# Kernel optimization log

Hardware: AMD Instinct MI355X
Metric: run time of the kernel (lower is better)

The kernel has to match this reference:

```python
import jax, jax.numpy as jnp
import numpy as np

B, N, D_IN = 256, 64, 128   # batch, n_agents, input_dim
H0, H1, H2 = 256, 256, 64   # rnn_hidden_dim[0], [1], [2]


def setup_inputs() -> dict:
    key = jax.random.key(0)
    ks = jax.random.split(key, 14)
    s = 0.05
    return {
        "obs": jax.random.normal(ks[0], (B, N, D_IN), dtype=jnp.float32),
        "W_enc": jax.random.normal(ks[1], (H0, D_IN), dtype=jnp.float32) * s,
        "b_enc": jax.random.normal(ks[2], (H0,), dtype=jnp.float32) * s,
        "W_obs": jax.random.normal(ks[3], (H0, H0), dtype=jnp.float32) * s,
        "b_obs": jax.random.normal(ks[4], (H0,), dtype=jnp.float32) * s,
        "W_ih": jax.random.normal(ks[5], (3 * H0, H0), dtype=jnp.float32) * s,
        "b_ih": jax.random.normal(ks[6], (3 * H0,), dtype=jnp.float32) * s,
        "W_hh": jax.random.normal(ks[7], (3 * H0, H0), dtype=jnp.float32) * s,
        "b_hh": jax.random.normal(ks[8], (3 * H0,), dtype=jnp.float32) * s,
        "W_val": jax.random.normal(ks[9], (H1, H0), dtype=jnp.float32) * s,
        "b_val": jax.random.normal(ks[10], (H1,), dtype=jnp.float32) * s,
        "W_dec": jax.random.normal(ks[11], (H2, H1), dtype=jnp.float32) * s,
        "b_dec": jax.random.normal(ks[12], (H2,), dtype=jnp.float32) * s,
    }


def reference(obs, W_enc, b_enc, W_obs, b_obs, W_ih, b_ih, W_hh, b_hh,
              W_val, b_val, W_dec, b_dec):
    # encoding + f_obs  -> h: [B, N, H0]
    x = jax.nn.relu(jnp.einsum("bnd,hd->bnh", obs, W_enc) + b_enc)
    h = jnp.einsum("bnh,gh->bng", x, W_obs) + b_obs

    # comm: mean over other agents. Original masks self and divides by N
    # (mean over dim of size N with self zeroed) => (sum_all - self) / N.
    c = (jnp.sum(h, axis=1, keepdims=True) - h) / N  # [B, N, H0]

    # GRUCell(input=c, hidden=h), PyTorch gate ordering r, z, n
    gi = jnp.einsum("bnh,gh->bng", c, W_ih) + b_ih   # [B, N, 3*H0]
    gh = jnp.einsum("bnh,gh->bng", h, W_hh) + b_hh
    gi_r, gi_z, gi_n = jnp.split(gi, 3, axis=-1)
    gh_r, gh_z, gh_n = jnp.split(gh, 3, axis=-1)
    r = jax.nn.sigmoid(gi_r + gh_r)
    z = jax.nn.sigmoid(gi_z + gh_z)
    n = jnp.tanh(gi_n + r * gh_n)
    h = (1.0 - z) * n + z * h  # [B, N, H0]

    # value head + decoding; seq_len=1 squeezed -> [B, N, H2]
    v = jnp.einsum("bnh,vh->bnv", h, W_val) + b_val
    out = jnp.einsum("bnv,ov->bno", v, W_dec) + b_dec
    return out
```

## Files before the change

kernel.cpp:

```cpp
#include <hip/hip_runtime.h>
#include <hip/hip_bf16.h>
#include <math.h>


typedef __bf16  bf16x8 __attribute__((ext_vector_type(8)));
typedef float   f32x4  __attribute__((ext_vector_type(4)));

#define DIN 128
#define H0  256
#define SW  264
#define SWO 136
#define LOG2E 1.44269504088896f

#define O_WENC  0
#define O_WOBS  32768
#define O_WIH   98304
#define O_WHH   294912
#define O_WFUSE 491520
#define W_CONV  491520
#define NBLK_CONV 240
#define O_BFUSE_B 1015808

__device__ __forceinline__ f32x4 mfma16(bf16x8 a, bf16x8 b, f32x4 c) {
    return __builtin_amdgcn_mfma_f32_16x16x32_bf16(a, b, c, 0, 0, 0);
}
__device__ __forceinline__ float bf2f(__hip_bfloat16 x) { return __bfloat162float(x); }
__device__ __forceinline__ __hip_bfloat16 f2bf(float x) { return __float2bfloat16(x); }

__device__ __forceinline__ float fsigmoid(float x) {
    float e = __builtin_amdgcn_exp2f(-LOG2E * x);
    return __builtin_amdgcn_rcpf(1.0f + e);
}
__device__ __forceinline__ float ftanh(float x) {
    float e = __builtin_amdgcn_exp2f(2.0f * LOG2E * x);
    return 1.0f - 2.0f * __builtin_amdgcn_rcpf(1.0f + e);
}

__device__ __forceinline__ bf16x8 w8(const __hip_bfloat16* p, int idx) {
    return *(const bf16x8*)(p + idx);
}

__device__ __forceinline__ int tadr(int r, int k) { return r * SW + k; }
__device__ __forceinline__ int oadr(int r, int k) { return r * SWO + k; }

__global__ __launch_bounds__(256) void prep_kernel(
    const float* __restrict__ W_enc, const float* __restrict__ W_obs,
    const float* __restrict__ W_ih,  const float* __restrict__ W_hh,
    const float* __restrict__ W_val, const float* __restrict__ W_dec,
    const float* __restrict__ b_val, const float* __restrict__ b_dec,
    __hip_bfloat16* __restrict__ ws)
{
    const int blk = blockIdx.x;
    const int tid = threadIdx.x;
    if (blk < NBLK_CONV) {
        const int i = (blk * 256 + tid) * 8;
        const float* src; int off;
        if      (i < O_WOBS) { src = W_enc; off = O_WENC; }
        else if (i < O_WIH)  { src = W_obs; off = O_WOBS; }
        else if (i < O_WHH)  { src = W_ih;  off = O_WIH;  }
        else                 { src = W_hh;  off = O_WHH;  }
        const float* f = src + (i - off);
        f32x4 a = *(const f32x4*)f;
        f32x4 b = *(const f32x4*)(f + 4);
        bf16x8 v;
        #pragma unroll
        for (int j = 0; j < 4; j++) { v[j] = (__bf16)a[j]; v[j + 4] = (__bf16)b[j]; }
        *(bf16x8*)(ws + i) = v;
    } else {
        const int o = blk - NBLK_CONV;
        __shared__ float wd[256];
        wd[tid] = W_dec[o * 256 + tid];
        __syncthreads();
        float acc = 0.0f;
        #pragma unroll 16
        for (int v = 0; v < 256; v++)
            acc += wd[v] * W_val[v * 256 + tid];
        ws[O_WFUSE + o * 256 + tid] = f2bf(acc);
        if (tid < 64) {
            float p = 0.0f;
            #pragma unroll
            for (int v = tid; v < 256; v += 64) p += wd[v] * b_val[v];
            p += __shfl_xor(p, 32); p += __shfl_xor(p, 16); p += __shfl_xor(p, 8);
            p += __shfl_xor(p, 4);  p += __shfl_xor(p, 2);  p += __shfl_xor(p, 1);
            if (tid == 0) {
                float* bf = (float*)((char*)ws + O_BFUSE_B);
                bf[o] = p + b_dec[o];
            }
        }
    }
}

__global__ __launch_bounds__(512, 2) void commnet_mfma(
    const __hip_bfloat16* __restrict__ ws,
    const float* __restrict__ b_enc, const float* __restrict__ b_obs,
    const float* __restrict__ b_ih,  const float* __restrict__ b_hh,
    const float* __restrict__ obs,   float* __restrict__ out)
{
    __shared__ __align__(16) __hip_bfloat16 T0[64 * SW];
    __shared__ __align__(16) __hip_bfloat16 T1[64 * SW];

    const __hip_bfloat16* W_enc  = ws + O_WENC;
    const __hip_bfloat16* W_obs  = ws + O_WOBS;
    const __hip_bfloat16* W_ih   = ws + O_WIH;
    const __hip_bfloat16* W_hh   = ws + O_WHH;
    const __hip_bfloat16* W_fuse = ws + O_WFUSE;
    const float* b_fuse = (const float*)((const char*)ws + O_BFUSE_B);

    const int tid  = threadIdx.x;
    const int wave = tid >> 6;
    const int lane = tid & 63;
    const int quad = lane >> 4;
    const int lc   = lane & 15;
    const int row0 = blockIdx.x * 64;
    const int ko16 = quad * 8;

    for (int i = tid; i < 64 * DIN / 8; i += 512) {
        const int r = i >> 4;
        const int c = (i & 15) << 3;
        const float* src = obs + (row0 + r) * DIN + c;
        f32x4 a = *(const f32x4*)src;
        f32x4 b = *(const f32x4*)(src + 4);
        bf16x8 v;
        #pragma unroll
        for (int j = 0; j < 4; j++) { v[j] = (__bf16)a[j]; v[j + 4] = (__bf16)b[j]; }
        *(bf16x8*)&T1[oadr(r, c)] = v;
    }
    __syncthreads();

    #pragma unroll
    for (int cp = 0; cp < 2; cp++) {
        const int n = (wave + 8 * cp) * 16 + lc;
        const float bias = b_enc[n];
        f32x4 acc[4] = {};
        #pragma unroll
        for (int k0 = 0; k0 < DIN; k0 += 32) {
            const int kk = k0 + ko16;
            bf16x8 b = w8(W_enc, n * DIN + kk);
            #pragma unroll
            for (int rt = 0; rt < 4; rt++) {
                bf16x8 a = *(const bf16x8*)&T1[oadr(rt * 16 + lc, kk)];
                acc[rt] = mfma16(a, b, acc[rt]);
            }
        }
        #pragma unroll
        for (int rt = 0; rt < 4; rt++)
            #pragma unroll
            for (int i = 0; i < 4; i++) {
                const int row = rt * 16 + quad * 4 + i;
                T0[tadr(row, n)] = f2bf(fmaxf(acc[rt][i] + bias, 0.0f));
            }
    }
    __syncthreads();

    #pragma unroll
    for (int cp = 0; cp < 2; cp++) {
        const int n = (wave + 8 * cp) * 16 + lc;
        const float bias = b_obs[n];
        f32x4 acc[4] = {};
        #pragma unroll
        for (int k0 = 0; k0 < H0; k0 += 32) {
            const int kk = k0 + ko16;
            bf16x8 b = w8(W_obs, n * H0 + kk);
            #pragma unroll
            for (int rt = 0; rt < 4; rt++) {
                bf16x8 a = *(const bf16x8*)&T0[tadr(rt * 16 + lc, kk)];
                acc[rt] = mfma16(a, b, acc[rt]);
            }
        }
        #pragma unroll
        for (int rt = 0; rt < 4; rt++)
            #pragma unroll
            for (int i = 0; i < 4; i++) {
                const int row = rt * 16 + quad * 4 + i;
                T1[tadr(row, n)] = f2bf(acc[rt][i] + bias);
            }
    }
    __syncthreads();

    #pragma unroll
    for (int cp = 0; cp < 2; cp++) {
        const int n = (wave + 8 * cp) * 16 + lc;
        const float bir = b_ih[n], biz = b_ih[n + 256], bin = b_ih[n + 512];
        const float bhr = b_hh[n], bhz = b_hh[n + 256], bhn = b_hh[n + 512];
        f32x4 gir[4] = {}, giz[4] = {}, gin[4] = {};
        f32x4 ghr[4] = {}, ghz[4] = {}, ghn[4] = {};
        #pragma unroll
        for (int k0 = 0; k0 < H0; k0 += 32) {
            const int kk = k0 + ko16;
            bf16x8 bir8 = w8(W_ih, (n      ) * H0 + kk);
            bf16x8 biz8 = w8(W_ih, (n + 256) * H0 + kk);
            bf16x8 bin8 = w8(W_ih, (n + 512) * H0 + kk);
            bf16x8 bhr8 = w8(W_hh, (n      ) * H0 + kk);
            bf16x8 bhz8 = w8(W_hh, (n + 256) * H0 + kk);
            bf16x8 bhn8 = w8(W_hh, (n + 512) * H0 + kk);
            #pragma unroll
            for (int rt = 0; rt < 4; rt++) {
                bf16x8 aH = *(const bf16x8*)&T1[tadr(rt * 16 + lc, kk)];
                gir[rt] = mfma16(aH, bir8, gir[rt]);
                giz[rt] = mfma16(aH, biz8, giz[rt]);
                gin[rt] = mfma16(aH, bin8, gin[rt]);
                ghr[rt] = mfma16(aH, bhr8, ghr[rt]);
                ghz[rt] = mfma16(aH, bhz8, ghz[rt]);
                ghn[rt] = mfma16(aH, bhn8, ghn[rt]);
            }
        }
        float Sr = 0.0f, Sz = 0.0f, Sn = 0.0f;
        #pragma unroll
        for (int rt = 0; rt < 4; rt++)
            #pragma unroll
            for (int i = 0; i < 4; i++) {
                Sr += gir[rt][i]; Sz += giz[rt][i]; Sn += gin[rt][i];
            }
        Sr += __shfl_xor(Sr, 16); Sr += __shfl_xor(Sr, 32);
        Sz += __shfl_xor(Sz, 16); Sz += __shfl_xor(Sz, 32);
        Sn += __shfl_xor(Sn, 16); Sn += __shfl_xor(Sn, 32);

        #pragma unroll
        for (int rt = 0; rt < 4; rt++)
            #pragma unroll
            for (int i = 0; i < 4; i++) {
                const int row = rt * 16 + quad * 4 + i;
                const float gi_r = (Sr - gir[rt][i]) * (1.0f / 64.0f) + bir;
                const float gi_z = (Sz - giz[rt][i]) * (1.0f / 64.0f) + biz;
                const float gi_n = (Sn - gin[rt][i]) * (1.0f / 64.0f) + bin;
                const float r  = fsigmoid(gi_r + ghr[rt][i] + bhr);
                const float z  = fsigmoid(gi_z + ghz[rt][i] + bhz);
                const float nn = ftanh(gi_n + r * (ghn[rt][i] + bhn));
                const float h  = bf2f(T1[tadr(row, n)]);
                T0[tadr(row, n)] = f2bf((1.0f - z) * nn + z * h);
            }
    }
    __syncthreads();

    {
        const int ct  = wave & 3;
        const int rtb = (wave >> 2) * 2;
        const int nd  = ct * 16 + lc;
        const float bias = b_fuse[nd];
        f32x4 acc[2] = {};
        #pragma unroll
        for (int k0 = 0; k0 < H0; k0 += 32) {
            const int kk = k0 + ko16;
            bf16x8 b = w8(W_fuse, nd * H0 + kk);
            #pragma unroll
            for (int j = 0; j < 2; j++) {
                bf16x8 a = *(const bf16x8*)&T0[tadr((rtb + j) * 16 + lc, kk)];
                acc[j] = mfma16(a, b, acc[j]);
            }
        }
        #pragma unroll
        for (int j = 0; j < 2; j++)
            #pragma unroll
            for (int i = 0; i < 4; i++) {
                const int row = (rtb + j) * 16 + quad * 4 + i;
                out[(row0 + row) * 64 + nd] = acc[j][i] + bias;
            }
    }
}

extern "C" void kernel_launch(void* const* d_in, const int* in_sizes, int n_in,
                              void* d_out, int out_size, void* d_ws, size_t ws_size,
                              hipStream_t stream) {
    (void)in_sizes; (void)n_in; (void)out_size; (void)ws_size;
    const float* obs   = (const float*)d_in[0];
    const float* W_enc = (const float*)d_in[1];  const float* b_enc = (const float*)d_in[2];
    const float* W_obs = (const float*)d_in[3];  const float* b_obs = (const float*)d_in[4];
    const float* W_ih  = (const float*)d_in[5];  const float* b_ih  = (const float*)d_in[6];
    const float* W_hh  = (const float*)d_in[7];  const float* b_hh  = (const float*)d_in[8];
    const float* W_val = (const float*)d_in[9];  const float* b_val = (const float*)d_in[10];
    const float* W_dec = (const float*)d_in[11]; const float* b_dec = (const float*)d_in[12];
    float* out = (float*)d_out;
    __hip_bfloat16* ws = (__hip_bfloat16*)d_ws;

    prep_kernel<<<NBLK_CONV + 64, 256, 0, stream>>>(
        W_enc, W_obs, W_ih, W_hh, W_val, W_dec, b_val, b_dec, ws);
    commnet_mfma<<<256, 512, 0, stream>>>(
        ws, b_enc, b_obs, b_ih, b_hh, obs, out);
}
```

Measured before the change: 126.5 us.

## Split fused kernel into two half-batch kernels exchanging h through workspace

The single 256-block kernel becomes two kernels with 512 blocks, each block handling 32 of a batch's 64 agents. Kernel A runs encoder and f_obs, writes h and per-half column sums to global workspace. Kernel B rebuilds the comm term from the column sums: it computes W_ih times the summed h as a scalar dot product and combines it with per-row W_ih·h, so the agent mean no longer needs all 64 rows in one block. This doubles block count for better CU occupancy, at the cost of an extra launch, a global round trip of h, and reloading weights twice as often per row.

New measurement: 194.5 us. 53.8% more time.

```diff
diff --git a/kernel.cpp b/kernel.cpp
--- a/kernel.cpp
+++ b/kernel.cpp
@@ -17,9 +17,10 @@
 #define O_WIH   98304
 #define O_WHH   294912
 #define O_WFUSE 491520
-#define W_CONV  491520
 #define NBLK_CONV 240
 #define O_BFUSE_B 1015808
+#define O_CS_B    1016320
+#define O_H_B     1540608
 
 __device__ __forceinline__ f32x4 mfma16(bf16x8 a, bf16x8 b, f32x4 c) {
     return __builtin_amdgcn_mfma_f32_16x16x32_bf16(a, b, c, 0, 0, 0);
@@ -90,39 +91,38 @@
     }
 }
 
-__global__ __launch_bounds__(512, 2) void commnet_mfma(
-    const __hip_bfloat16* __restrict__ ws,
+__global__ __launch_bounds__(512, 2) void commnet_a(
+    __hip_bfloat16* __restrict__ ws,
     const float* __restrict__ b_enc, const float* __restrict__ b_obs,
-    const float* __restrict__ b_ih,  const float* __restrict__ b_hh,
-    const float* __restrict__ obs,   float* __restrict__ out)
+    const float* __restrict__ obs)
 {
-    __shared__ __align__(16) __hip_bfloat16 T0[64 * SW];
-    __shared__ __align__(16) __hip_bfloat16 T1[64 * SW];
-
-    const __hip_bfloat16* W_enc  = ws + O_WENC;
-    const __hip_bfloat16* W_obs  = ws + O_WOBS;
-    const __hip_bfloat16* W_ih   = ws + O_WIH;
-    const __hip_bfloat16* W_hh   = ws + O_WHH;
-    const __hip_bfloat16* W_fuse = ws + O_WFUSE;
-    const float* b_fuse = (const float*)((const char*)ws + O_BFUSE_B);
+    __shared__ __align__(16) __hip_bfloat16 T0[32 * SW];
+    __shared__ __align__(16) __hip_bfloat16 T1[32 * SW];
+
+    const __hip_bfloat16* W_enc = ws + O_WENC;
+    const __hip_bfloat16* W_obs = ws + O_WOBS;
+    float* cs = (float*)((char*)ws + O_CS_B);
+    __hip_bfloat16* Hb = (__hip_bfloat16*)((char*)ws + O_H_B);
 
     const int tid  = threadIdx.x;
     const int wave = tid >> 6;
     const int lane = tid & 63;
     const int quad = lane >> 4;
     const int lc   = lane & 15;
-    const int row0 = blockIdx.x * 64;
+    const int b    = blockIdx.x >> 1;
+    const int half = blockIdx.x & 1;
+    const int r0g  = b * 64 + half * 32;
     const int ko16 = quad * 8;
 
-    for (int i = tid; i < 64 * DIN / 8; i += 512) {
-        const int r = i >> 4;
-        const int c = (i & 15) << 3;
-        const float* src = obs + (row0 + r) * DIN + c;
+    {
+        const int r = tid >> 4;
+        const int c = (tid & 15) << 3;
+        const float* src = obs + (r0g + r) * DIN + c;
         f32x4 a = *(const f32x4*)src;
-        f32x4 b = *(const f32x4*)(src + 4);
+        f32x4 bq = *(const f32x4*)(src + 4);
         bf16x8 v;
         #pragma unroll
-        for (int j = 0; j < 4; j++) { v[j] = (__bf16)a[j]; v[j + 4] = (__bf16)b[j]; }
+        for (int j = 0; j < 4; j++) { v[j] = (__bf16)a[j]; v[j + 4] = (__bf16)bq[j]; }
         *(bf16x8*)&T1[oadr(r, c)] = v;
     }
     __syncthreads();
@@ -131,19 +131,19 @@
     for (int cp = 0; cp < 2; cp++) {
         const int n = (wave + 8 * cp) * 16 + lc;
         const float bias = b_enc[n];
-        f32x4 acc[4] = {};
+        f32x4 acc[2] = {};
         #pragma unroll
         for (int k0 = 0; k0 < DIN; k0 += 32) {
             const int kk = k0 + ko16;
-            bf16x8 b = w8(W_enc, n * DIN + kk);
-            #pragma unroll
-            for (int rt = 0; rt < 4; rt++) {
+            bf16x8 bw = w8(W_enc, n * DIN + kk);
+            #pragma unroll
+            for (int rt = 0; rt < 2; rt++) {
                 bf16x8 a = *(const bf16x8*)&T1[oadr(rt * 16 + lc, kk)];
-                acc[rt] = mfma16(a, b, acc[rt]);
-            }
-        }
-        #pragma unroll
-        for (int rt = 0; rt < 4; rt++)
+                acc[rt] = mfma16(a, bw, acc[rt]);
+            }
+        }
+        #pragma unroll
+        for (int rt = 0; rt < 2; rt++)
             #pragma unroll
             for (int i = 0; i < 4; i++) {
                 const int row = rt * 16 + quad * 4 + i;
@@ -156,35 +156,101 @@
     for (int cp = 0; cp < 2; cp++) {
         const int n = (wave + 8 * cp) * 16 + lc;
         const float bias = b_obs[n];
-        f32x4 acc[4] = {};
-        #pragma unroll
+        f32x4 acc[2] = {};
+        #pragma unroll 4
         for (int k0 = 0; k0 < H0; k0 += 32) {
             const int kk = k0 + ko16;
-            bf16x8 b = w8(W_obs, n * H0 + kk);
-            #pragma unroll
-            for (int rt = 0; rt < 4; rt++) {
+            bf16x8 bw = w8(W_obs, n * H0 + kk);
+            #pragma unroll
+            for (int rt = 0; rt < 2; rt++) {
                 bf16x8 a = *(const bf16x8*)&T0[tadr(rt * 16 + lc, kk)];
-                acc[rt] = mfma16(a, b, acc[rt]);
-            }
-        }
-        #pragma unroll
-        for (int rt = 0; rt < 4; rt++)
+                acc[rt] = mfma16(a, bw, acc[rt]);
+            }
+        }
+        float Sc = 0.0f;
+        #pragma unroll
+        for (int rt = 0; rt < 2; rt++)
             #pragma unroll
             for (int i = 0; i < 4; i++) {
                 const int row = rt * 16 + quad * 4 + i;
-                T1[tadr(row, n)] = f2bf(acc[rt][i] + bias);
-            }
-    }
+                const __hip_bfloat16 hb = f2bf(acc[rt][i] + bias);
+                T1[tadr(row, n)] = hb;
+                Sc += bf2f(hb);
+            }
+        Sc += __shfl_xor(Sc, 16); Sc += __shfl_xor(Sc, 32);
+        if (lane < 16) cs[blockIdx.x * 256 + n] = Sc;
+    }
+    __syncthreads();
+
+    for (int i = tid; i < 32 * H0 / 8; i += 512) {
+        const int r = i >> 5;
+        const int c = (i & 31) << 3;
+        *(bf16x8*)&Hb[(r0g + r) * H0 + c] = *(const bf16x8*)&T1[tadr(r, c)];
+    }
+}
+
+__global__ __launch_bounds__(512, 2) void commnet_b(
+    __hip_bfloat16* __restrict__ ws,
+    const float* __restrict__ b_ih, const float* __restrict__ b_hh,
+    float* __restrict__ out)
+{
+    __shared__ __align__(16) __hip_bfloat16 T0[32 * SW];
+    __shared__ __align__(16) __hip_bfloat16 T1[32 * SW];
+    __shared__ float Ls[256];
+
+    const __hip_bfloat16* W_ih   = ws + O_WIH;
+    const __hip_bfloat16* W_hh   = ws + O_WHH;
+    const __hip_bfloat16* W_fuse = ws + O_WFUSE;
+    const float* b_fuse = (const float*)((const char*)ws + O_BFUSE_B);
+    const float* cs = (const float*)((const char*)ws + O_CS_B);
+    const __hip_bfloat16* Hb = (const __hip_bfloat16*)((const char*)ws + O_H_B);
+
+    const int tid  = threadIdx.x;
+    const int wave = tid >> 6;
+    const int lane = tid & 63;
+    const int quad = lane >> 4;
+    const int lc   = lane & 15;
+    const int b    = blockIdx.x >> 1;
+    const int half = blockIdx.x & 1;
+    const int r0g  = b * 64 + half * 32;
+    const int ko16 = quad * 8;
+
+    for (int i = tid; i < 32 * H0 / 8; i += 512) {
+        const int r = i >> 5;
+        const int c = (i & 31) << 3;
+        *(bf16x8*)&T1[tadr(r, c)] = *(const bf16x8*)&Hb[(r0g + r) * H0 + c];
+    }
+    if (tid < 256)
+        Ls[tid] = cs[(b * 2) * 256 + tid] + cs[(b * 2 + 1) * 256 + tid];
     __syncthreads();
 
     #pragma unroll
     for (int cp = 0; cp < 2; cp++) {
         const int n = (wave + 8 * cp) * 16 + lc;
+        float Sr = 0.0f, Sz = 0.0f, Sn = 0.0f;
+        #pragma unroll
+        for (int j0 = 0; j0 < 64; j0 += 8) {
+            const int k = quad * 64 + j0;
+            bf16x8 wr = w8(W_ih, (n      ) * H0 + k);
+            bf16x8 wz = w8(W_ih, (n + 256) * H0 + k);
+            bf16x8 wn = w8(W_ih, (n + 512) * H0 + k);
+            #pragma unroll
+            for (int t = 0; t < 8; t++) {
+                const float sv = Ls[k + t];
+                Sr += sv * (float)wr[t];
+                Sz += sv * (float)wz[t];
+                Sn += sv * (float)wn[t];
+            }
+        }
+        Sr += __shfl_xor(Sr, 16); Sr += __shfl_xor(Sr, 32);
+        Sz += __shfl_xor(Sz, 16); Sz += __shfl_xor(Sz, 32);
+        Sn += __shfl_xor(Sn, 16); Sn += __shfl_xor(Sn, 32);
+
         const float bir = b_ih[n], biz = b_ih[n + 256], bin = b_ih[n + 512];
         const float bhr = b_hh[n], bhz = b_hh[n + 256], bhn = b_hh[n + 512];
-        f32x4 gir[4] = {}, giz[4] = {}, gin[4] = {};
-        f32x4 ghr[4] = {}, ghz[4] = {}, ghn[4] = {};
-        #pragma unroll
+        f32x4 gir[2] = {}, giz[2] = {}, gin[2] = {};
+        f32x4 ghr[2] = {}, ghz[2] = {}, ghn[2] = {};
+        #pragma unroll 4
         for (int k0 = 0; k0 < H0; k0 += 32) {
             const int kk = k0 + ko16;
             bf16x8 bir8 = w8(W_ih, (n      ) * H0 + kk);
@@ -194,7 +260,7 @@
             bf16x8 bhz8 = w8(W_hh, (n + 256) * H0 + kk);
             bf16x8 bhn8 = w8(W_hh, (n + 512) * H0 + kk);
             #pragma unroll
-            for (int rt = 0; rt < 4; rt++) {
+            for (int rt = 0; rt < 2; rt++) {
                 bf16x8 aH = *(const bf16x8*)&T1[tadr(rt * 16 + lc, kk)];
                 gir[rt] = mfma16(aH, bir8, gir[rt]);
                 giz[rt] = mfma16(aH, biz8, giz[rt]);
@@ -204,19 +270,8 @@
                 ghn[rt] = mfma16(aH, bhn8, ghn[rt]);
             }
         }
-        float Sr = 0.0f, Sz = 0.0f, Sn = 0.0f;
-        #pragma unroll
-        for (int rt = 0; rt < 4; rt++)
-            #pragma unroll
-            for (int i = 0; i < 4; i++) {
-                Sr += gir[rt][i]; Sz += giz[rt][i]; Sn += gin[rt][i];
-            }
-        Sr += __shfl_xor(Sr, 16); Sr += __shfl_xor(Sr, 32);
-        Sz += __shfl_xor(Sz, 16); Sz += __shfl_xor(Sz, 32);
-        Sn += __shfl_xor(Sn, 16); Sn += __shfl_xor(Sn, 32);
-
-        #pragma unroll
-        for (int rt = 0; rt < 4; rt++)
+        #pragma unroll
+        for (int rt = 0; rt < 2; rt++)
             #pragma unroll
             for (int i = 0; i < 4; i++) {
                 const int row = rt * 16 + quad * 4 + i;
@@ -233,28 +288,23 @@
     __syncthreads();
 
     {
-        const int ct  = wave & 3;
-        const int rtb = (wave >> 2) * 2;
-        const int nd  = ct * 16 + lc;
+        const int ct = wave & 3;
+        const int rt = wave >> 2;
+        const int nd = ct * 16 + lc;
         const float bias = b_fuse[nd];
-        f32x4 acc[2] = {};
-        #pragma unroll
+        f32x4 acc = {};
+        #pragma unroll 4
         for (int k0 = 0; k0 < H0; k0 += 32) {
             const int kk = k0 + ko16;
-            bf16x8 b = w8(W_fuse, nd * H0 + kk);
-            #pragma unroll
-            for (int j = 0; j < 2; j++) {
-                bf16x8 a = *(const bf16x8*)&T0[tadr((rtb + j) * 16 + lc, kk)];
-                acc[j] = mfma16(a, b, acc[j]);
-            }
-        }
-        #pragma unroll
-        for (int j = 0; j < 2; j++)
-            #pragma unroll
-            for (int i = 0; i < 4; i++) {
-                const int row = (rtb + j) * 16 + quad * 4 + i;
-                out[(row0 + row) * 64 + nd] = acc[j][i] + bias;
-            }
+            bf16x8 bw = w8(W_fuse, nd * H0 + kk);
+            bf16x8 a = *(const bf16x8*)&T0[tadr(rt * 16 + lc, kk)];
+            acc = mfma16(a, bw, acc);
+        }
+        #pragma unroll
+        for (int i = 0; i < 4; i++) {
+            const int row = rt * 16 + quad * 4 + i;
+            out[(r0g + row) * 64 + nd] = acc[i] + bias;
+        }
     }
 }
 
@@ -274,6 +324,6 @@
 
     prep_kernel<<<NBLK_CONV + 64, 256, 0, stream>>>(
         W_enc, W_obs, W_ih, W_hh, W_val, W_dec, b_val, b_dec, ws);
-    commnet_mfma<<<256, 512, 0, stream>>>(
-        ws, b_enc, b_obs, b_ih, b_hh, obs, out);
-}
+    commnet_a<<<512, 512, 0, stream>>>(ws, b_enc, b_obs, obs);
+    commnet_b<<<512, 512, 0, stream>>>(ws, b_ih, b_hh, out);
+}
```
